# Optimization experiments

Hardware: AMD Instinct MI355X
Metric: run time of the kernel (lower is better)

Reference implementation:

```python
import jax, jax.numpy as jnp
import numpy as np

B, S, DM = 2, 2048, 1024
H, D = 16, 64  # multiheads, head_dim; H*D == DM
NEG = -1e9


def setup_inputs() -> dict:
    key = jax.random.key(0)
    ks = jax.random.split(key, 7)
    xavier = float(np.sqrt(6.0 / (DM + H * D)))
    return {
        "Q": jax.random.normal(ks[0], (B, S, DM), dtype=jnp.float32),
        "K": jax.random.normal(ks[1], (B, S, DM), dtype=jnp.float32),
        "V": jax.random.normal(ks[2], (B, S, DM), dtype=jnp.float32),
        "V_len": jax.random.randint(ks[3], (B,), 0, S),
        "WQ": jax.random.uniform(ks[4], (DM, H * D), dtype=jnp.float32, minval=-xavier, maxval=xavier),
        "WK": jax.random.uniform(ks[5], (DM, H * D), dtype=jnp.float32, minval=-xavier, maxval=xavier),
        "WV": jax.random.uniform(ks[6], (DM, H * D), dtype=jnp.float32, minval=-xavier, maxval=xavier),
    }


def reference(Q, K, V, V_len, WQ, WK, WV):
    b, s, _ = Q.shape
    # project and split heads: [B,S,DM] -> [B,H,S,D]
    q = (Q @ WQ).reshape(b, s, H, D).transpose(0, 2, 1, 3)
    k = (K @ WK).reshape(b, s, H, D).transpose(0, 2, 1, 3)
    v = (V @ WV).reshape(b, s, H, D).transpose(0, 2, 1, 3)
    scores = jnp.einsum("bhqd,bhkd->bhqk", q, k) / jnp.sqrt(jnp.float32(D))
    # key padding mask: valid keys are positions < V_len[b]
    valid = jnp.arange(s)[None, :] < V_len[:, None]          # [B,S]
    scores = jnp.where(valid[:, None, None, :], scores, NEG)  # [B,H,Sq,Sk]
    attn = jax.nn.softmax(scores, axis=-1)
    out = jnp.einsum("bhqk,bhkd->bhqd", attn, v)
    return out.transpose(0, 2, 1, 3).reshape(b, s, H * D)
```

## Files before the change

kernel.cpp:

```cpp
#include <hip/hip_runtime.h>
#include <hip/hip_bf16.h>

#define NBATCH 2
#define SEQ 2048
#define DMODEL 1024
#define NHEAD 16
#define HDIM 64
#define ROWS (NBATCH*SEQ)

typedef __attribute__((ext_vector_type(8))) short bf16x8;
typedef __attribute__((ext_vector_type(4))) float f32x4;
typedef __attribute__((ext_vector_type(16))) float f32x16;

#define MFMA16 __builtin_amdgcn_mfma_f32_16x16x32_bf16
#define MFMA32 __builtin_amdgcn_mfma_f32_32x32x16_bf16

#define QSCALE 0.1803368801111204f

static __device__ __forceinline__ unsigned short f2bf(float f) {
    unsigned int u = __float_as_uint(f);
    u += 0x7fffu + ((u >> 16) & 1u);
    return (unsigned short)(u >> 16);
}

static __device__ __forceinline__ unsigned cvtpk(float lo, float hi) {
    unsigned r;
    asm("v_cvt_pk_bf16_f32 %0, %1, %2" : "=v"(r) : "v"(lo), "v"(hi));
    return r;
}

static __device__ __forceinline__ void gld16(const unsigned short* g, unsigned short* l) {
    __builtin_amdgcn_global_load_lds(
        (const __attribute__((address_space(1))) unsigned int*)g,
        (__attribute__((address_space(3))) unsigned int*)l,
        16, 0, 0);
}

__global__ __launch_bounds__(256) void cvt_kernel(const float* __restrict__ Q, const float* __restrict__ K,
                                                  const float* __restrict__ V, const int* __restrict__ vlenp,
                                                  const float* __restrict__ W0, const float* __restrict__ W1,
                                                  const float* __restrict__ W2,
                                                  unsigned short* __restrict__ dq, unsigned short* __restrict__ dk,
                                                  unsigned short* __restrict__ dv,
                                                  unsigned short* __restrict__ T0, unsigned short* __restrict__ T1,
                                                  unsigned short* __restrict__ T2, int n8) {
    __shared__ float tile[64][65];
    const int z = blockIdx.z;
    const int tid = threadIdx.x;
    if (z == 3) {
        const int bx = blockIdx.x;
        if (bx >= 768) return;
        const int mat = bx >> 8, idx = bx & 255;
        const float* W = mat == 0 ? W0 : (mat == 1 ? W1 : W2);
        unsigned short* T = mat == 0 ? T0 : (mat == 1 ? T1 : T2);
        int rb = (idx >> 4) * 64, cb = (idx & 15) * 64;
        #pragma unroll
        for (int rep = 0; rep < 16; ++rep) {
            int i = rep * 256 + tid; int r = i >> 6, c = i & 63;
            tile[r][c] = W[(size_t)(rb + r) * DMODEL + cb + c];
        }
        __syncthreads();
        #pragma unroll
        for (int rep = 0; rep < 16; ++rep) {
            int i = rep * 256 + tid; int r = i >> 6, c = i & 63;
            T[(size_t)(cb + r) * DMODEL + rb + c] = f2bf(tile[c][r]);
        }
        return;
    }
    int i = blockIdx.x * 256 + tid;
    if (i >= n8) return;
    if (z) {
        int row = i >> 7;
        int bb = row >> 11, s = row & 2047;
        int vl = vlenp[bb];
        int lim = ((vl + 31) >> 5) << 5;
        if (z == 1) { if (vl == 0 || s >= lim) return; }
        else        { if (vl != 0 && s >= lim) return; }
    }
    const float* src = z == 0 ? Q : (z == 1 ? K : V);
    unsigned short* dst = z == 0 ? dq : (z == 1 ? dk : dv);
    const float4* s4 = (const float4*)src;
    float4 a = s4[2 * i], b = s4[2 * i + 1];
    union { bf16x8 v; unsigned short u[8]; } o;
    o.u[0] = f2bf(a.x); o.u[1] = f2bf(a.y); o.u[2] = f2bf(a.z); o.u[3] = f2bf(a.w);
    o.u[4] = f2bf(b.x); o.u[5] = f2bf(b.y); o.u[6] = f2bf(b.z); o.u[7] = f2bf(b.w);
    *(bf16x8*)(dst + (size_t)i * 8) = o.v;
}

__global__ __launch_bounds__(512) void proj_kernel(
        const unsigned short* __restrict__ Xq, const unsigned short* __restrict__ Xk,
        const unsigned short* __restrict__ Xv,
        const unsigned short* __restrict__ WTq, const unsigned short* __restrict__ WTk,
        const unsigned short* __restrict__ WTv, const int* __restrict__ vlenp,
        unsigned short* __restrict__ qp, unsigned short* __restrict__ kp,
        unsigned short* __restrict__ vtp) {
    const int mode = blockIdx.z;
    const int lin = blockIdx.y * gridDim.x + blockIdx.x;
    const int xcd = lin & 7, chunk = lin >> 3;
    const int by2 = (chunk >> 3) * 8 + xcd;
    const int bx2 = chunk & 7;
    const int rowBase = by2 * 128;
    const int colBase = bx2 * 128;

    if (mode >= 1) {
        const int bb = rowBase >> 11, sS = rowBase & 2047;
        const int vl = vlenp[bb];
        const int lim = ((vl + 31) >> 5) << 5;
        if (mode == 1) { if (vl == 0 || sS >= lim) return; }
        else           { if (vl != 0 && sS >= lim) return; }
    }

    const unsigned short* X  = mode == 0 ? Xq  : (mode == 1 ? Xk  : Xv);
    const unsigned short* WT = mode == 0 ? WTq : (mode == 1 ? WTk : WTv);

    __shared__ unsigned short As[2][128 * 64];
    __shared__ unsigned short Bs[2][128 * 64];

    const int tid = threadIdx.x, lane = tid & 63, w = tid >> 6;
    const int wr = w >> 2, wc = w & 3;

    const int rloc = lane >> 3;
    const int ssw  = ((lane & 7) * 8) ^ (rloc * 8);

    f32x4 acc[4][2];
    #pragma unroll
    for (int i = 0; i < 4; ++i)
        #pragma unroll
        for (int j = 0; j < 2; ++j) acc[i][j] = (f32x4){0.f, 0.f, 0.f, 0.f};

    for (int kt = 0; kt < DMODEL / 128; ++kt) {
        #pragma unroll
        for (int hf = 0; hf < 2; ++hf)
            #pragma unroll
            for (int j = 0; j < 2; ++j) {
                int c = w * 2 + j;
                int r = c * 8 + rloc;
                gld16(X  + (size_t)(rowBase + r) * DMODEL + kt * 128 + hf * 64 + ssw, &As[hf][c * 512]);
                gld16(WT + (size_t)(colBase + r) * DMODEL + kt * 128 + hf * 64 + ssw, &Bs[hf][c * 512]);
            }
        __syncthreads();

        #pragma unroll
        for (int hf = 0; hf < 2; ++hf) {
            const char* Ab = (const char*)(mode < 2 ? &As[hf][0] : &Bs[hf][0]);
            const char* Bb = (const char*)(mode < 2 ? &Bs[hf][0] : &As[hf][0]);
            #pragma unroll
            for (int ks = 0; ks < 2; ++ks) {
                const int kbyte = ks * 64 + ((lane >> 4) * 16);
                bf16x8 af[4], bfr[2];
                #pragma unroll
                for (int i = 0; i < 4; ++i) {
                    int ar = wr * 64 + i * 16 + (lane & 15);
                    af[i] = *(const bf16x8*)(Ab + ar * 128 + (kbyte ^ ((ar & 7) << 4)));
                }
                #pragma unroll
                for (int j = 0; j < 2; ++j) {
                    int br = wc * 32 + j * 16 + (lane & 15);
                    bfr[j] = *(const bf16x8*)(Bb + br * 128 + (kbyte ^ ((br & 7) << 4)));
                }
                #pragma unroll
                for (int i = 0; i < 4; ++i)
                    #pragma unroll
                    for (int j = 0; j < 2; ++j)
                        acc[i][j] = MFMA16(af[i], bfr[j], acc[i][j], 0, 0, 0);
            }
        }
        __syncthreads();
    }

    if (mode < 2) {
        unsigned short* outp = (mode == 0) ? qp : kp;
        const float sc = (mode == 0) ? QSCALE : 1.0f;
        #pragma unroll
        for (int i = 0; i < 4; ++i)
            #pragma unroll
            for (int j = 0; j < 2; ++j)
                #pragma unroll
                for (int r = 0; r < 4; ++r) {
                    int grow = rowBase + wr * 64 + i * 16 + (lane >> 4) * 4 + r;
                    int gcol = colBase + wc * 32 + j * 16 + (lane & 15);
                    int b = grow >> 11, s = grow & 2047, hh = gcol >> 6, d = gcol & 63;
                    outp[((size_t)(b * NHEAD + hh) * SEQ + s) * HDIM + d] = f2bf(acc[i][j][r] * sc);
                }
    } else {
        #pragma unroll
        for (int i = 0; i < 4; ++i)
            #pragma unroll
            for (int j = 0; j < 2; ++j)
                #pragma unroll
                for (int r = 0; r < 4; ++r) {
                    int gcol = colBase + wr * 64 + i * 16 + (lane >> 4) * 4 + r;
                    int grow = rowBase + wc * 32 + j * 16 + (lane & 15);
                    int b = grow >> 11, s = grow & 2047, hh = gcol >> 6, d = gcol & 63;
                    vtp[((size_t)(b * NHEAD + hh) * HDIM + d) * SEQ + s] = f2bf(acc[i][j][r]);
                }
    }
}

__global__ __launch_bounds__(256, 4) void attn_kernel(
        const unsigned short* __restrict__ qp, const unsigned short* __restrict__ kp,
        const unsigned short* __restrict__ vtp, const int* __restrict__ vlenp,
        float* __restrict__ out) {
    const int tid = threadIdx.x, lane = tid & 63, w = tid >> 6;
    const int hh = lane >> 5;
    const int ql = lane & 31;
    const int qsub = w >> 1, kpar = w & 1;
    const int qt = blockIdx.x, h = blockIdx.y, b = blockIdx.z;
    const int vlen = vlenp[b];
    const int nt = (vlen == 0) ? (SEQ / 32) : ((vlen + 31) >> 5);
    const int myn = (nt - kpar + 1) >> 1;
    const int J = (nt + 1) >> 1;
    const float maskval = (vlen == 0) ? 0.0f : -1e9f;

    __shared__ unsigned short Kd[2][2][2048];
    __shared__ unsigned short Vd[2][2][2048];
    __shared__ float mlb[4][32];

    const size_t headQ = (size_t)(b * NHEAD + h) * SEQ * HDIM;
    const size_t headV = (size_t)(b * NHEAD + h) * HDIM * SEQ;

    const int qrow = qt * 64 + qsub * 32 + ql;
    bf16x8 qf[4];
    #pragma unroll
    for (int ks = 0; ks < 4; ++ks)
        qf[ks] = *(const bf16x8*)(qp + headQ + (size_t)qrow * HDIM + ks * 16 + hh * 8);

    f32x16 o0, o1;
    #pragma unroll
    for (int r = 0; r < 16; ++r) { o0[r] = 0.f; o1[r] = 0.f; }
    float l_run = 0.f;

    const int rloc = lane >> 3;
    const int ssw  = ((lane & 7) * 8) ^ (rloc * 8);
    const int gn   = (lane & 7) ^ rloc;
    const int koff = (gn & 3) * 8;
    const int dhi  = (gn >> 2) * 32;

    auto stageK = [&](int kvB, int buf) {
        #pragma unroll
        for (int c = 0; c < 4; ++c)
            gld16(kp + headQ + (size_t)(kvB + c * 8 + rloc) * HDIM + ssw, &Kd[kpar][buf][c * 512]);
    };
    auto stageV = [&](int kvB, int buf) {
        #pragma unroll
        for (int c = 0; c < 4; ++c)
            gld16(vtp + headV + (size_t)(c * 8 + rloc + dhi) * SEQ + kvB + koff, &Vd[kpar][buf][c * 512]);
    };

    if (myn > 0) { if (qsub == 0) stageK(kpar * 32, 0); else stageV(kpar * 32, 0); }

    for (int j = 0; j < J; ++j) {
        const int cur = j & 1;
        __syncthreads();

        if (j + 1 < myn) {
            const int nb = (kpar + 2 * (j + 1)) * 32;
            if (qsub == 0) stageK(nb, cur ^ 1); else stageV(nb, cur ^ 1);
        }

        if (j < myn) {
            const int kvBase = (kpar + 2 * j) * 32;
            const char* Kb = (const char*)&Kd[kpar][cur][0];
            const char* Vb = (const char*)&Vd[kpar][cur][0];

            f32x16 s0;
            #pragma unroll
            for (int r = 0; r < 16; ++r) s0[r] = 0.f;
            __builtin_amdgcn_s_setprio(1);
            #pragma unroll
            for (int ks = 0; ks < 4; ++ks) {
                const int kb = (ks * 32 + hh * 16) ^ ((ql & 7) << 4);
                bf16x8 kf = *(const bf16x8*)(Kb + ql * 128 + kb);
                s0 = MFMA32(kf, qf[ks], s0, 0, 0, 0);
            }
            __builtin_amdgcn_s_setprio(0);

            if (kvBase + 32 > vlen) {
                #pragma unroll
                for (int r = 0; r < 16; ++r) {
                    int kl = (r & 3) + 8 * (r >> 2) + 4 * hh;
                    if (kvBase + kl >= vlen) s0[r] = maskval;
                }
            }

            #pragma unroll
            for (int r = 0; r < 16; ++r) s0[r] = __builtin_amdgcn_exp2f(s0[r]);
            float sm[8];
            #pragma unroll
            for (int t = 0; t < 8; ++t) sm[t] = s0[t] + s0[t + 8];
            #pragma unroll
            for (int st = 4; st > 0; st >>= 1)
                #pragma unroll
                for (int t = 0; t < st; ++t) sm[t] += sm[t + st];
            l_run += sm[0] + __shfl_xor(sm[0], 32);

            unsigned d0[8];
            #pragma unroll
            for (int t = 0; t < 8; ++t) d0[t] = cvtpk(s0[2 * t], s0[2 * t + 1]);

            __builtin_amdgcn_s_setprio(1);
#define PV_SLICE(KSL)                                                              \
            {                                                                      \
                unsigned a0 = d0[4 * (KSL)],     b0 = d0[4 * (KSL) + 2];           \
                unsigned a1 = d0[4 * (KSL) + 1], b1 = d0[4 * (KSL) + 3];           \
                asm("v_permlane32_swap_b32 %0, %1" : "+v"(a0), "+v"(b0));          \
                asm("v_permlane32_swap_b32 %0, %1" : "+v"(a1), "+v"(b1));          \
                union { unsigned u[4]; bf16x8 v; } pa;                             \
                pa.u[0] = a0; pa.u[1] = a1; pa.u[2] = b0; pa.u[3] = b1;            \
                const int gA = 2 * (KSL) + hh;                                     \
                bf16x8 vfA = *(const bf16x8*)(Vb + ql * 128 + ((gA ^ (ql & 7)) << 4));        \
                bf16x8 vfB = *(const bf16x8*)(Vb + ql * 128 + (((4 + gA) ^ (ql & 7)) << 4));  \
                o0 = MFMA32(vfA, pa.v, o0, 0, 0, 0);                               \
                o1 = MFMA32(vfB, pa.v, o1, 0, 0, 0);                               \
            }
            PV_SLICE(0)
            PV_SLICE(1)
#undef PV_SLICE
            __builtin_amdgcn_s_setprio(0);
        }
    }

    if (hh == 0) mlb[w][ql] = l_run;
    __syncthreads();
    if (kpar == 1) {
        char* Ob = ((char*)Kd) + qsub * 8192;
        #pragma unroll
        for (int g = 0; g < 4; ++g) {
            int ad = ql * 256 + ((32 * g + 16 * hh) ^ (16 * (ql & 7)));
            *(float4*)(Ob + ad)       = make_float4(o0[4*g], o0[4*g+1], o0[4*g+2], o0[4*g+3]);
            *(float4*)(Ob + ad + 128) = make_float4(o1[4*g], o1[4*g+1], o1[4*g+2], o1[4*g+3]);
        }
    }
    __syncthreads();
    if (kpar == 0) {
        const float lp = mlb[w + 1][ql];
        const float linv = 1.0f / (l_run + lp);
        const char* Pb = ((const char*)Kd) + qsub * 8192;
        float* orow = out + (size_t)(b * SEQ + qrow) * DMODEL + h * HDIM;
        #pragma unroll
        for (int g = 0; g < 4; ++g) {
            int ad = ql * 256 + ((32 * g + 16 * hh) ^ (16 * (ql & 7)));
            float4 p0 = *(const float4*)(Pb + ad);
            float4 p1 = *(const float4*)(Pb + ad + 128);
            *(float4*)(orow + 8 * g + 4 * hh) = make_float4(
                (o0[4*g]   + p0.x) * linv, (o0[4*g+1] + p0.y) * linv,
                (o0[4*g+2] + p0.z) * linv, (o0[4*g+3] + p0.w) * linv);
            *(float4*)(orow + 32 + 8 * g + 4 * hh) = make_float4(
                (o1[4*g]   + p1.x) * linv, (o1[4*g+1] + p1.y) * linv,
                (o1[4*g+2] + p1.z) * linv, (o1[4*g+3] + p1.w) * linv);
        }
    }
}

extern "C" void kernel_launch(void* const* d_in, const int* in_sizes, int n_in,
                              void* d_out, int out_size, void* d_ws, size_t ws_size,
                              hipStream_t stream) {
    const float* Q  = (const float*)d_in[0];
    const float* K  = (const float*)d_in[1];
    const float* V  = (const float*)d_in[2];
    const int* V_len = (const int*)d_in[3];
    const float* WQ = (const float*)d_in[4];
    const float* WK = (const float*)d_in[5];
    const float* WV = (const float*)d_in[6];
    float* out = (float*)d_out;

    char* ws = (char*)d_ws;
    const size_t MB = 1024 * 1024;
    unsigned short* Xq  = (unsigned short*)(ws + 0 * MB);
    unsigned short* Xk  = (unsigned short*)(ws + 8 * MB);
    unsigned short* Xv  = (unsigned short*)(ws + 16 * MB);
    unsigned short* WTq = (unsigned short*)(ws + 24 * MB);
    unsigned short* WTk = (unsigned short*)(ws + 26 * MB);
    unsigned short* WTv = (unsigned short*)(ws + 28 * MB);
    unsigned short* qpj = (unsigned short*)(ws + 30 * MB);
    unsigned short* kpj = (unsigned short*)(ws + 38 * MB);
    unsigned short* vtp = (unsigned short*)(ws + 46 * MB);

    const int n8 = ROWS * DMODEL / 8;
    cvt_kernel<<<dim3((n8 + 255) / 256, 1, 4), 256, 0, stream>>>(
        Q, K, V, V_len, WQ, WK, WV, Xq, Xk, Xv, WTq, WTk, WTv, n8);
    proj_kernel<<<dim3(8, 32, 3), 512, 0, stream>>>(
        Xq, Xk, Xv, WTq, WTk, WTv, V_len, qpj, kpj, vtp);
    attn_kernel<<<dim3(SEQ / 64, NHEAD, NBATCH), 256, 0, stream>>>(qpj, kpj, vtp, V_len, out);
}
```

Before: 77.87 us.

## Widen projection GEMM tile to 128x256 and double-buffer K-loop loads

```diff
diff --git a/kernel.cpp b/kernel.cpp
--- a/kernel.cpp
+++ b/kernel.cpp
@@ -97,10 +97,10 @@
     const int mode = blockIdx.z;
     const int lin = blockIdx.y * gridDim.x + blockIdx.x;
     const int xcd = lin & 7, chunk = lin >> 3;
-    const int by2 = (chunk >> 3) * 8 + xcd;
-    const int bx2 = chunk & 7;
+    const int by2 = (chunk >> 2) * 8 + xcd;
+    const int bx2 = chunk & 3;
     const int rowBase = by2 * 128;
-    const int colBase = bx2 * 128;
+    const int colBase = bx2 * 256;
 
     if (mode >= 1) {
         const int bb = rowBase >> 11, sS = rowBase & 2047;
@@ -114,58 +114,67 @@
     const unsigned short* WT = mode == 0 ? WTq : (mode == 1 ? WTk : WTv);
 
     __shared__ unsigned short As[2][128 * 64];
-    __shared__ unsigned short Bs[2][128 * 64];
+    __shared__ unsigned short Bs[2][256 * 64];
 
     const int tid = threadIdx.x, lane = tid & 63, w = tid >> 6;
-    const int wr = w >> 2, wc = w & 3;
+    const int wA = (mode < 2) ? (w >> 2) : (w & 3);
+    const int wB = (mode < 2) ? (w & 3) : (w >> 2);
 
     const int rloc = lane >> 3;
     const int ssw  = ((lane & 7) * 8) ^ (rloc * 8);
 
-    f32x4 acc[4][2];
+    f32x4 acc[4][4];
     #pragma unroll
     for (int i = 0; i < 4; ++i)
         #pragma unroll
-        for (int j = 0; j < 2; ++j) acc[i][j] = (f32x4){0.f, 0.f, 0.f, 0.f};
-
-    for (int kt = 0; kt < DMODEL / 128; ++kt) {
-        #pragma unroll
-        for (int hf = 0; hf < 2; ++hf)
-            #pragma unroll
-            for (int j = 0; j < 2; ++j) {
-                int c = w * 2 + j;
-                int r = c * 8 + rloc;
-                gld16(X  + (size_t)(rowBase + r) * DMODEL + kt * 128 + hf * 64 + ssw, &As[hf][c * 512]);
-                gld16(WT + (size_t)(colBase + r) * DMODEL + kt * 128 + hf * 64 + ssw, &Bs[hf][c * 512]);
-            }
+        for (int j = 0; j < 4; ++j) acc[i][j] = (f32x4){0.f, 0.f, 0.f, 0.f};
+
+    auto stage = [&](int kt, int buf) {
+        #pragma unroll
+        for (int j = 0; j < 2; ++j) {
+            int c = w * 2 + j;
+            int r = c * 8 + rloc;
+            gld16(X + (size_t)(rowBase + r) * DMODEL + kt * 64 + ssw, &As[buf][c * 512]);
+        }
+        #pragma unroll
+        for (int j = 0; j < 4; ++j) {
+            int c = w * 4 + j;
+            int r = c * 8 + rloc;
+            gld16(WT + (size_t)(colBase + r) * DMODEL + kt * 64 + ssw, &Bs[buf][c * 512]);
+        }
+    };
+
+    stage(0, 0);
+
+    for (int kt = 0; kt < DMODEL / 64; ++kt) {
+        const int cur = kt & 1;
         __syncthreads();
 
-        #pragma unroll
-        for (int hf = 0; hf < 2; ++hf) {
-            const char* Ab = (const char*)(mode < 2 ? &As[hf][0] : &Bs[hf][0]);
-            const char* Bb = (const char*)(mode < 2 ? &Bs[hf][0] : &As[hf][0]);
-            #pragma unroll
-            for (int ks = 0; ks < 2; ++ks) {
-                const int kbyte = ks * 64 + ((lane >> 4) * 16);
-                bf16x8 af[4], bfr[2];
-                #pragma unroll
-                for (int i = 0; i < 4; ++i) {
-                    int ar = wr * 64 + i * 16 + (lane & 15);
-                    af[i] = *(const bf16x8*)(Ab + ar * 128 + (kbyte ^ ((ar & 7) << 4)));
-                }
-                #pragma unroll
-                for (int j = 0; j < 2; ++j) {
-                    int br = wc * 32 + j * 16 + (lane & 15);
-                    bfr[j] = *(const bf16x8*)(Bb + br * 128 + (kbyte ^ ((br & 7) << 4)));
-                }
-                #pragma unroll
-                for (int i = 0; i < 4; ++i)
-                    #pragma unroll
-                    for (int j = 0; j < 2; ++j)
-                        acc[i][j] = MFMA16(af[i], bfr[j], acc[i][j], 0, 0, 0);
-            }
-        }
-        __syncthreads();
+        if (kt + 1 < DMODEL / 64) stage(kt + 1, cur ^ 1);
+
+        const char* Ab = (const char*)(mode < 2 ? &As[cur][0] : &Bs[cur][0]);
+        const char* Bb = (const char*)(mode < 2 ? &Bs[cur][0] : &As[cur][0]);
+
+        #pragma unroll
+        for (int ks = 0; ks < 2; ++ks) {
+            const int kbyte = ks * 64 + ((lane >> 4) * 16);
+            bf16x8 af[4], bfr[4];
+            #pragma unroll
+            for (int i = 0; i < 4; ++i) {
+                int ar = wA * 64 + i * 16 + (lane & 15);
+                af[i] = *(const bf16x8*)(Ab + ar * 128 + (kbyte ^ ((ar & 7) << 4)));
+            }
+            #pragma unroll
+            for (int j = 0; j < 4; ++j) {
+                int br = wB * 64 + j * 16 + (lane & 15);
+                bfr[j] = *(const bf16x8*)(Bb + br * 128 + (kbyte ^ ((br & 7) << 4)));
+            }
+            #pragma unroll
+            for (int i = 0; i < 4; ++i)
+                #pragma unroll
+                for (int j = 0; j < 4; ++j)
+                    acc[i][j] = MFMA16(af[i], bfr[j], acc[i][j], 0, 0, 0);
+        }
     }
 
     if (mode < 2) {
@@ -174,11 +183,11 @@
         #pragma unroll
         for (int i = 0; i < 4; ++i)
             #pragma unroll
-            for (int j = 0; j < 2; ++j)
+            for (int j = 0; j < 4; ++j)
                 #pragma unroll
                 for (int r = 0; r < 4; ++r) {
-                    int grow = rowBase + wr * 64 + i * 16 + (lane >> 4) * 4 + r;
-                    int gcol = colBase + wc * 32 + j * 16 + (lane & 15);
+                    int grow = rowBase + wA * 64 + i * 16 + (lane >> 4) * 4 + r;
+                    int gcol = colBase + wB * 64 + j * 16 + (lane & 15);
                     int b = grow >> 11, s = grow & 2047, hh = gcol >> 6, d = gcol & 63;
                     outp[((size_t)(b * NHEAD + hh) * SEQ + s) * HDIM + d] = f2bf(acc[i][j][r] * sc);
                 }
@@ -186,11 +195,11 @@
         #pragma unroll
         for (int i = 0; i < 4; ++i)
             #pragma unroll
-            for (int j = 0; j < 2; ++j)
+            for (int j = 0; j < 4; ++j)
                 #pragma unroll
                 for (int r = 0; r < 4; ++r) {
-                    int gcol = colBase + wr * 64 + i * 16 + (lane >> 4) * 4 + r;
-                    int grow = rowBase + wc * 32 + j * 16 + (lane & 15);
+                    int gcol = colBase + wA * 64 + i * 16 + (lane >> 4) * 4 + r;
+                    int grow = rowBase + wB * 64 + j * 16 + (lane & 15);
                     int b = grow >> 11, s = grow & 2047, hh = gcol >> 6, d = gcol & 63;
                     vtp[((size_t)(b * NHEAD + hh) * HDIM + d) * SEQ + s] = f2bf(acc[i][j][r]);
                 }
@@ -379,7 +388,7 @@
     const int n8 = ROWS * DMODEL / 8;
     cvt_kernel<<<dim3((n8 + 255) / 256, 1, 4), 256, 0, stream>>>(
         Q, K, V, V_len, WQ, WK, WV, Xq, Xk, Xv, WTq, WTk, WTv, n8);
-    proj_kernel<<<dim3(8, 32, 3), 512, 0, stream>>>(
+    proj_kernel<<<dim3(4, 32, 3), 512, 0, stream>>>(
         Xq, Xk, Xv, WTq, WTk, WTv, V_len, qpj, kpj, vtp);
     attn_kernel<<<dim3(SEQ / 64, NHEAD, NBATCH), 256, 0, stream>>>(qpj, kpj, vtp, V_len, out);
 }
```

Result: slower. 90.26 us (+15.9%).

## Fuse fp32-to-bf16 activation conversion into projection GEMM loads

Applied to the files above, without the earlier changes.

```diff
diff --git a/kernel.cpp b/kernel.cpp
--- a/kernel.cpp
+++ b/kernel.cpp
@@ -35,61 +35,39 @@
         (__attribute__((address_space(3))) unsigned int*)l,
         16, 0, 0);
 }
-
-__global__ __launch_bounds__(256) void cvt_kernel(const float* __restrict__ Q, const float* __restrict__ K,
-                                                  const float* __restrict__ V, const int* __restrict__ vlenp,
-                                                  const float* __restrict__ W0, const float* __restrict__ W1,
-                                                  const float* __restrict__ W2,
-                                                  unsigned short* __restrict__ dq, unsigned short* __restrict__ dk,
-                                                  unsigned short* __restrict__ dv,
-                                                  unsigned short* __restrict__ T0, unsigned short* __restrict__ T1,
-                                                  unsigned short* __restrict__ T2, int n8) {
+static __device__ __forceinline__ void gld16f(const float* g, float* l) {
+    __builtin_amdgcn_global_load_lds(
+        (const __attribute__((address_space(1))) unsigned int*)g,
+        (__attribute__((address_space(3))) unsigned int*)l,
+        16, 0, 0);
+}
+
+__global__ __launch_bounds__(256) void wtrans_kernel(const float* __restrict__ W0, const float* __restrict__ W1,
+                                                     const float* __restrict__ W2,
+                                                     unsigned short* __restrict__ T0, unsigned short* __restrict__ T1,
+                                                     unsigned short* __restrict__ T2) {
     __shared__ float tile[64][65];
-    const int z = blockIdx.z;
+    const int bx = blockIdx.x;
+    const int mat = bx >> 8, idx = bx & 255;
+    const float* W = mat == 0 ? W0 : (mat == 1 ? W1 : W2);
+    unsigned short* T = mat == 0 ? T0 : (mat == 1 ? T1 : T2);
+    const int rb = (idx >> 4) * 64, cb = (idx & 15) * 64;
     const int tid = threadIdx.x;
-    if (z == 3) {
-        const int bx = blockIdx.x;
-        if (bx >= 768) return;
-        const int mat = bx >> 8, idx = bx & 255;
-        const float* W = mat == 0 ? W0 : (mat == 1 ? W1 : W2);
-        unsigned short* T = mat == 0 ? T0 : (mat == 1 ? T1 : T2);
-        int rb = (idx >> 4) * 64, cb = (idx & 15) * 64;
-        #pragma unroll
-        for (int rep = 0; rep < 16; ++rep) {
-            int i = rep * 256 + tid; int r = i >> 6, c = i & 63;
-            tile[r][c] = W[(size_t)(rb + r) * DMODEL + cb + c];
-        }
-        __syncthreads();
-        #pragma unroll
-        for (int rep = 0; rep < 16; ++rep) {
-            int i = rep * 256 + tid; int r = i >> 6, c = i & 63;
-            T[(size_t)(cb + r) * DMODEL + rb + c] = f2bf(tile[c][r]);
-        }
-        return;
-    }
-    int i = blockIdx.x * 256 + tid;
-    if (i >= n8) return;
-    if (z) {
-        int row = i >> 7;
-        int bb = row >> 11, s = row & 2047;
-        int vl = vlenp[bb];
-        int lim = ((vl + 31) >> 5) << 5;
-        if (z == 1) { if (vl == 0 || s >= lim) return; }
-        else        { if (vl != 0 && s >= lim) return; }
-    }
-    const float* src = z == 0 ? Q : (z == 1 ? K : V);
-    unsigned short* dst = z == 0 ? dq : (z == 1 ? dk : dv);
-    const float4* s4 = (const float4*)src;
-    float4 a = s4[2 * i], b = s4[2 * i + 1];
-    union { bf16x8 v; unsigned short u[8]; } o;
-    o.u[0] = f2bf(a.x); o.u[1] = f2bf(a.y); o.u[2] = f2bf(a.z); o.u[3] = f2bf(a.w);
-    o.u[4] = f2bf(b.x); o.u[5] = f2bf(b.y); o.u[6] = f2bf(b.z); o.u[7] = f2bf(b.w);
-    *(bf16x8*)(dst + (size_t)i * 8) = o.v;
+    #pragma unroll
+    for (int rep = 0; rep < 16; ++rep) {
+        int i = rep * 256 + tid; int r = i >> 6, c = i & 63;
+        tile[r][c] = W[(size_t)(rb + r) * DMODEL + cb + c];
+    }
+    __syncthreads();
+    #pragma unroll
+    for (int rep = 0; rep < 16; ++rep) {
+        int i = rep * 256 + tid; int r = i >> 6, c = i & 63;
+        T[(size_t)(cb + r) * DMODEL + rb + c] = f2bf(tile[c][r]);
+    }
 }
 
 __global__ __launch_bounds__(512) void proj_kernel(
-        const unsigned short* __restrict__ Xq, const unsigned short* __restrict__ Xk,
-        const unsigned short* __restrict__ Xv,
+        const float* __restrict__ Xq, const float* __restrict__ Xk, const float* __restrict__ Xv,
         const unsigned short* __restrict__ WTq, const unsigned short* __restrict__ WTk,
         const unsigned short* __restrict__ WTv, const int* __restrict__ vlenp,
         unsigned short* __restrict__ qp, unsigned short* __restrict__ kp,
@@ -110,17 +88,19 @@
         else           { if (vl != 0 && sS >= lim) return; }
     }
 
-    const unsigned short* X  = mode == 0 ? Xq  : (mode == 1 ? Xk  : Xv);
+    const float* X = mode == 0 ? Xq : (mode == 1 ? Xk : Xv);
     const unsigned short* WT = mode == 0 ? WTq : (mode == 1 ? WTk : WTv);
 
-    __shared__ unsigned short As[2][128 * 64];
-    __shared__ unsigned short Bs[2][128 * 64];
+    __shared__ float As[128 * 64];
+    __shared__ unsigned short Bs[128 * 64];
 
     const int tid = threadIdx.x, lane = tid & 63, w = tid >> 6;
     const int wr = w >> 2, wc = w & 3;
 
-    const int rloc = lane >> 3;
-    const int ssw  = ((lane & 7) * 8) ^ (rloc * 8);
+    const int rlocB = lane >> 3;
+    const int sswB  = ((lane & 7) * 8) ^ (rlocB * 8);
+    const int rlA = lane >> 4;
+    const int uA  = lane & 15;
 
     f32x4 acc[4][2];
     #pragma unroll
@@ -128,42 +108,56 @@
         #pragma unroll
         for (int j = 0; j < 2; ++j) acc[i][j] = (f32x4){0.f, 0.f, 0.f, 0.f};
 
-    for (int kt = 0; kt < DMODEL / 128; ++kt) {
-        #pragma unroll
-        for (int hf = 0; hf < 2; ++hf)
-            #pragma unroll
-            for (int j = 0; j < 2; ++j) {
-                int c = w * 2 + j;
-                int r = c * 8 + rloc;
-                gld16(X  + (size_t)(rowBase + r) * DMODEL + kt * 128 + hf * 64 + ssw, &As[hf][c * 512]);
-                gld16(WT + (size_t)(colBase + r) * DMODEL + kt * 128 + hf * 64 + ssw, &Bs[hf][c * 512]);
+    auto ldA = [&](int ar, int ks) -> bf16x8 {
+        const int u0 = ks * 8 + (lane >> 4) * 2;
+        const float* rowp = &As[ar * 64];
+        float4 f0 = *(const float4*)(rowp + ((u0 ^ (ar & 15)) * 4));
+        float4 f1 = *(const float4*)(rowp + (((u0 + 1) ^ (ar & 15)) * 4));
+        union { unsigned u[4]; bf16x8 v; } t;
+        t.u[0] = cvtpk(f0.x, f0.y); t.u[1] = cvtpk(f0.z, f0.w);
+        t.u[2] = cvtpk(f1.x, f1.y); t.u[3] = cvtpk(f1.z, f1.w);
+        return t.v;
+    };
+    auto ldB = [&](int br, int ks) -> bf16x8 {
+        const int kbyte = ks * 64 + ((lane >> 4) * 16);
+        return *(const bf16x8*)((const char*)Bs + br * 128 + (kbyte ^ ((br & 7) << 4)));
+    };
+
+    for (int kt = 0; kt < DMODEL / 64; ++kt) {
+        #pragma unroll
+        for (int j = 0; j < 4; ++j) {
+            int c = w * 4 + j;
+            int r = c * 4 + rlA;
+            gld16f(X + (size_t)(rowBase + r) * DMODEL + kt * 64 + ((uA ^ (r & 15)) * 4),
+                   &As[c * 256]);
+        }
+        #pragma unroll
+        for (int j = 0; j < 2; ++j) {
+            int c = w * 2 + j;
+            int r = c * 8 + rlocB;
+            gld16(WT + (size_t)(colBase + r) * DMODEL + kt * 64 + sswB, &Bs[c * 512]);
+        }
+        __syncthreads();
+
+        #pragma unroll
+        for (int ks = 0; ks < 2; ++ks) {
+            bf16x8 af[4], bfr[2];
+            if (mode < 2) {
+                #pragma unroll
+                for (int i = 0; i < 4; ++i) af[i]  = ldA(wr * 64 + i * 16 + (lane & 15), ks);
+                #pragma unroll
+                for (int j = 0; j < 2; ++j) bfr[j] = ldB(wc * 32 + j * 16 + (lane & 15), ks);
+            } else {
+                #pragma unroll
+                for (int i = 0; i < 4; ++i) af[i]  = ldB(wr * 64 + i * 16 + (lane & 15), ks);
+                #pragma unroll
+                for (int j = 0; j < 2; ++j) bfr[j] = ldA(wc * 32 + j * 16 + (lane & 15), ks);
             }
-        __syncthreads();
-
-        #pragma unroll
-        for (int hf = 0; hf < 2; ++hf) {
-            const char* Ab = (const char*)(mode < 2 ? &As[hf][0] : &Bs[hf][0]);
-            const char* Bb = (const char*)(mode < 2 ? &Bs[hf][0] : &As[hf][0]);
-            #pragma unroll
-            for (int ks = 0; ks < 2; ++ks) {
-                const int kbyte = ks * 64 + ((lane >> 4) * 16);
-                bf16x8 af[4], bfr[2];
-                #pragma unroll
-                for (int i = 0; i < 4; ++i) {
-                    int ar = wr * 64 + i * 16 + (lane & 15);
-                    af[i] = *(const bf16x8*)(Ab + ar * 128 + (kbyte ^ ((ar & 7) << 4)));
-                }
-                #pragma unroll
-                for (int j = 0; j < 2; ++j) {
-                    int br = wc * 32 + j * 16 + (lane & 15);
-                    bfr[j] = *(const bf16x8*)(Bb + br * 128 + (kbyte ^ ((br & 7) << 4)));
-                }
-                #pragma unroll
-                for (int i = 0; i < 4; ++i)
-                    #pragma unroll
-                    for (int j = 0; j < 2; ++j)
-                        acc[i][j] = MFMA16(af[i], bfr[j], acc[i][j], 0, 0, 0);
-            }
+            #pragma unroll
+            for (int i = 0; i < 4; ++i)
+                #pragma unroll
+                for (int j = 0; j < 2; ++j)
+                    acc[i][j] = MFMA16(af[i], bfr[j], acc[i][j], 0, 0, 0);
         }
         __syncthreads();
     }
@@ -366,9 +360,6 @@
 
     char* ws = (char*)d_ws;
     const size_t MB = 1024 * 1024;
-    unsigned short* Xq  = (unsigned short*)(ws + 0 * MB);
-    unsigned short* Xk  = (unsigned short*)(ws + 8 * MB);
-    unsigned short* Xv  = (unsigned short*)(ws + 16 * MB);
     unsigned short* WTq = (unsigned short*)(ws + 24 * MB);
     unsigned short* WTk = (unsigned short*)(ws + 26 * MB);
     unsigned short* WTv = (unsigned short*)(ws + 28 * MB);
@@ -376,10 +367,8 @@
     unsigned short* kpj = (unsigned short*)(ws + 38 * MB);
     unsigned short* vtp = (unsigned short*)(ws + 46 * MB);
 
-    const int n8 = ROWS * DMODEL / 8;
-    cvt_kernel<<<dim3((n8 + 255) / 256, 1, 4), 256, 0, stream>>>(
-        Q, K, V, V_len, WQ, WK, WV, Xq, Xk, Xv, WTq, WTk, WTv, n8);
+    wtrans_kernel<<<dim3(768), 256, 0, stream>>>(WQ, WK, WV, WTq, WTk, WTv);
     proj_kernel<<<dim3(8, 32, 3), 512, 0, stream>>>(
-        Xq, Xk, Xv, WTq, WTk, WTv, V_len, qpj, kpj, vtp);
+        Q, K, V, WTq, WTk, WTv, V_len, qpj, kpj, vtp);
     attn_kernel<<<dim3(SEQ / 64, NHEAD, NBATCH), 256, 0, stream>>>(qpj, kpj, vtp, V_len, out);
 }
```

Result: slower. 84.33 us (+8.3%).
